# Kernel tuning notes

Measured on AMD Instinct MI355X. Metric: run time of the kernel, lower is better.

The kernel has to match this reference:

```python
import jax, jax.numpy as jnp
import numpy as np

N_NODES = 100000
N_EDGES = 1600000
N_HEADS = 4
D_IN = 128
D_OUT = 32


def setup_inputs() -> dict:
    key = jax.random.key(0)
    k1, k2, k3, k4, k5 = jax.random.split(key, 5)
    # glorot-ish scaling for params
    w_scale = (2.0 / (D_IN + D_OUT)) ** 0.5
    a_scale = (2.0 / (D_OUT + 1)) ** 0.5
    return {
        "H_in": jax.random.normal(k1, (N_NODES, D_IN), dtype=jnp.float32),
        "edge_index": jax.random.randint(k2, (2, N_EDGES), 0, N_NODES, dtype=jnp.int64),
        "W": jax.random.normal(k3, (N_HEADS, D_OUT, D_IN), dtype=jnp.float32) * w_scale,
        "A_src": jax.random.normal(k4, (N_HEADS, D_OUT), dtype=jnp.float32) * a_scale,
        "A_tgt": jax.random.normal(k5, (N_HEADS, D_OUT), dtype=jnp.float32) * a_scale,
    }


def reference(H_in, edge_index, W, A_src, A_tgt):
    # GATLayer.forward with dropout=0, skip=False, reduce='none', act=elu
    N = H_in.shape[0]
    src = edge_index[0]  # [E]
    tgt = edge_index[1]  # [E]

    # H_w: [N_h, N, D_out]  (einsum 'ij, nkj -> nik' in source)
    H_w = jnp.einsum("nd,hod->hno", H_in, W)

    # Per-node attention logit halves, then gather per edge (same math as
    # gathering features first and dotting with A afterwards).
    s_src = jnp.einsum("hno,ho->hn", H_w, A_src)  # [N_h, N]
    s_tgt = jnp.einsum("hno,ho->hn", H_w, A_tgt)  # [N_h, N]
    E_pre = s_src[:, src] + s_tgt[:, tgt]          # [N_h, E]
    E = jax.nn.leaky_relu(E_pre, negative_slope=0.2)

    # Segment softmax over edges grouped by target node (numerically stable).
    seg_max = jax.ops.segment_max(E.T, tgt, num_segments=N)  # [N, N_h]
    E_exp = jnp.exp(E - seg_max.T[:, tgt])                    # [N_h, E]
    seg_sum = jax.ops.segment_sum(E_exp.T, tgt, num_segments=N)  # [N, N_h]
    alpha = E_exp / seg_sum.T[:, tgt]                         # [N_h, E]

    # Weighted scatter-sum aggregation: msg [N_h, E, D_out] -> [N_h, N, D_out]
    msg = alpha[..., None] * H_w[:, src]
    H_out_pre = jax.vmap(lambda m: jax.ops.segment_sum(m, tgt, num_segments=N))(msg)

    return jax.nn.elu(H_out_pre)  # [N_h, N, D_out]
```

## Files before the change

### kernel.cpp

```cpp
#include <hip/hip_runtime.h>


#define CHUNK 4096
#define CAP 8192

typedef __attribute__((ext_vector_type(8))) short short8_t;
typedef __attribute__((ext_vector_type(4))) float float4v;
typedef __attribute__((ext_vector_type(2))) float float2v;

static __device__ inline float bf2f(unsigned short u) {
    return __uint_as_float(((unsigned int)u) << 16);
}
static __device__ inline unsigned short f2bf(float f) {
    unsigned int u = __float_as_uint(f);
    return (unsigned short)((u + 0x7fffu + ((u >> 16) & 1u)) >> 16);
}
static __device__ inline void splitf(float v, unsigned short& h, unsigned short& l) {
    unsigned short hb = f2bf(v);
    h = hb;
    l = f2bf(v - bf2f(hb));
}

__device__ inline int block_excl_scan(int v) {
    __shared__ int wsum[8];
    int lane = threadIdx.x & 63, w = threadIdx.x >> 6;
    int inc = v;
    for (int d = 1; d < 64; d <<= 1) {
        int t = __shfl_up(inc, d, 64);
        if (lane >= d) inc += t;
    }
    if (lane == 63) wsum[w] = inc;
    __syncthreads();
    int base = 0;
    for (int i = 0; i < w; ++i) base += wsum[i];
    __syncthreads();
    return base + inc - v;
}

__global__ __launch_bounds__(256) void k_scatA(const int* __restrict__ raw,
                                               int* __restrict__ cnt,
                                               unsigned int* __restrict__ pairs,
                                               int E, int N, int NB) {
    __shared__ unsigned int pl[CHUNK];
    __shared__ unsigned short bl[CHUNK];
    __shared__ int h[512];
    __shared__ int s_i64;
    const int tid = threadIdx.x;
    for (int i = tid; i < 512; i += 256) h[i] = 0;
    if (tid < 64) {
        unsigned int hiw = ((const unsigned int*)raw)[2 * tid + 1];
        unsigned long long b = __ballot(hiw == 0u);
        if (tid == 0) s_i64 = (__popcll(b) >= 32) ? 1 : 0;
    }
    __syncthreads();
    const bool i64 = s_i64 != 0;
    const int eBeg = blockIdx.x * CHUNK;
    const int eEnd = min(E, eBeg + CHUNK);
    const int cntE = eEnd - eBeg;
    for (int j = tid; j < cntE; j += 256) {
        int i = eBeg + j;
        int s, t;
        if (i64) {
            s = raw[2 * (size_t)i];
            t = raw[2 * ((size_t)E + i)];
        } else {
            s = raw[(size_t)i];
            t = raw[(size_t)E + i];
        }
        s = s < 0 ? 0 : (s >= N ? N - 1 : s);
        t = t < 0 ? 0 : (t >= N ? N - 1 : t);
        pl[j] = (unsigned)s | ((unsigned)(t & 255) << 24);
        int b = t >> 8;
        bl[j] = (unsigned short)b;
        atomicAdd(&h[b], 1);
    }
    __syncthreads();
    for (int b = tid; b < NB; b += 256) {
        int c = h[b];
        if (c > 0) h[b] = b * CAP + atomicAdd(&cnt[b], c);
    }
    __syncthreads();
    for (int j = tid; j < cntE; j += 256) {
        int slot = atomicAdd(&h[bl[j]], 1);
        pairs[slot] = pl[j];
    }
}

__global__ __launch_bounds__(256) void k_locs(const unsigned int* __restrict__ pairs,
                                              const int* __restrict__ cnt,
                                              int* __restrict__ offs,
                                              int* __restrict__ csr, int N, int NB,
                                              int E) {
    __shared__ int dcnt[256], cur[256];
    __shared__ int rsum[4];
    const int b = blockIdx.x;
    const int tid = threadIdx.x;

    int part = 0;
    for (int j = tid; j < b; j += 256) part += cnt[j];
    for (int d = 1; d < 64; d <<= 1) part += __shfl_xor(part, d, 64);
    if ((tid & 63) == 0) rsum[tid >> 6] = part;
    __syncthreads();
    const int obase = rsum[0] + rsum[1] + rsum[2] + rsum[3];

    const int c = cnt[b];
    const int rbeg = b * CAP;
    const int nodeBase = b << 8;
    dcnt[tid] = 0;
    __syncthreads();
    for (int i = tid; i < c; i += 256) atomicAdd(&dcnt[pairs[rbeg + i] >> 24], 1);
    __syncthreads();
    int v = dcnt[tid];
    int e = block_excl_scan(v);
    int n = nodeBase + tid;
    if (n < N) offs[n] = obase + e;
    cur[tid] = obase + e;
    __syncthreads();
    for (int i = tid; i < c; i += 256) {
        unsigned p = pairs[rbeg + i];
        int slot = atomicAdd(&cur[p >> 24], 1);
        csr[slot] = (int)(p & 0x00FFFFFFu);
    }
    if (b == 0 && tid == 0) offs[N] = E;
}

__global__ __launch_bounds__(256) void k_hw(const float* __restrict__ Hf,
                                            const float* __restrict__ Wf,
                                            const float* __restrict__ Asrc,
                                            const float* __restrict__ Atgt,
                                            unsigned short* __restrict__ Hwb,
                                            float* __restrict__ s_src,
                                            float* __restrict__ s_tgt, int nnodes) {
    __shared__ __align__(16) unsigned short Wh[64 * 136];
    __shared__ __align__(16) unsigned short Sh[16 * 136];
    __shared__ __align__(16) unsigned short Sl[16 * 136];
    __shared__ float sAs[128], sAt[128];

    int wave = threadIdx.x >> 6;
    int lane = threadIdx.x & 63;
    int mrow = lane & 15;
    int quad = lane >> 4;

    if (threadIdx.x < 128) {
        sAs[threadIdx.x] = Asrc[threadIdx.x];
        sAt[threadIdx.x] = Atgt[threadIdx.x];
    }
    __syncthreads();

    for (int i = threadIdx.x; i < 512; i += 256) {
        int r = i >> 5, c4 = (i & 31) * 4;
        float4v v = {0.f, 0.f, 0.f, 0.f};
        if (r < 8) {
            int hh_ = r & 3;
            const float* Ap = (r < 4) ? sAs : sAt;
            for (int o = 0; o < 32; ++o) {
                float4v w4 = *(const float4v*)(Wf + ((size_t)(hh_ * 32 + o)) * 128 + c4);
                float a = Ap[hh_ * 32 + o];
                v[0] += w4[0] * a;
                v[1] += w4[1] * a;
                v[2] += w4[2] * a;
                v[3] += w4[3] * a;
            }
        }
        ushort4 h4, l4;
        unsigned short hh, ll;
        splitf(v[0], hh, ll); h4.x = hh; l4.x = ll;
        splitf(v[1], hh, ll); h4.y = hh; l4.y = ll;
        splitf(v[2], hh, ll); h4.z = hh; l4.z = ll;
        splitf(v[3], hh, ll); h4.w = hh; l4.w = ll;
        *(ushort4*)&Sh[r * 136 + c4] = h4;
        *(ushort4*)&Sl[r * 136 + c4] = l4;
    }

    const float4v* wsrc = (const float4v*)Wf;

    for (int hb = 0; hb < 2; ++hb) {
        if (hb) __syncthreads();
        for (int i = threadIdx.x; i < 2048; i += 256) {
            int r = i >> 5, c4 = (i & 31) * 4;
            float4v v = wsrc[(hb * 64 + r) * 32 + (i & 31)];
            ushort4 h4;
            h4.x = f2bf(v[0]);
            h4.y = f2bf(v[1]);
            h4.z = f2bf(v[2]);
            h4.w = f2bf(v[3]);
            *(ushort4*)&Wh[r * 136 + c4] = h4;
        }
        __syncthreads();

        for (int nh = 0; nh < 2; ++nh) {
            int nbase = blockIdx.x * 128 + (wave * 2 + nh) * 16;
            if (nbase >= nnodes) continue;
            int anode = nbase + mrow;
            int nclamp = anode < nnodes ? anode : nnodes - 1;
            const float* Hp = Hf + (size_t)nclamp * 128 + quad * 8;

            float4v acc[4] = {};
            float4v accS = {};
            for (int kc = 0; kc < 4; ++kc) {
                float4v va = *(const float4v*)(Hp + kc * 32);
                float4v vb = *(const float4v*)(Hp + kc * 32 + 4);
                short8_t ah;
                ah[0] = (short)f2bf(va[0]);
                ah[1] = (short)f2bf(va[1]);
                ah[2] = (short)f2bf(va[2]);
                ah[3] = (short)f2bf(va[3]);
                ah[4] = (short)f2bf(vb[0]);
                ah[5] = (short)f2bf(vb[1]);
                ah[6] = (short)f2bf(vb[2]);
                ah[7] = (short)f2bf(vb[3]);
                for (int t = 0; t < 4; ++t) {
                    int boff = (t * 16 + mrow) * 136 + kc * 32 + quad * 8;
                    short8_t bh = *(const short8_t*)&Wh[boff];
                    acc[t] = __builtin_amdgcn_mfma_f32_16x16x32_bf16(ah, bh, acc[t], 0, 0, 0);
                }
                if (hb == 0) {
                    int soff = mrow * 136 + kc * 32 + quad * 8;
                    short8_t sh = *(const short8_t*)&Sh[soff];
                    short8_t sl = *(const short8_t*)&Sl[soff];
                    accS = __builtin_amdgcn_mfma_f32_16x16x32_bf16(ah, sh, accS, 0, 0, 0);
                    accS = __builtin_amdgcn_mfma_f32_16x16x32_bf16(ah, sl, accS, 0, 0, 0);
                }
            }
            for (int t = 0; t < 4; ++t)
                for (int r = 0; r < 4; ++r) {
                    int nrow = nbase + quad * 4 + r;
                    if (nrow < nnodes)
                        Hwb[(size_t)nrow * 128 + hb * 64 + t * 16 + mrow] = f2bf(acc[t][r]);
                }
            if (hb == 0) {
                for (int r = 0; r < 4; ++r) {
                    int nrow = nbase + quad * 4 + r;
                    if (nrow < nnodes) {
                        if (mrow < 4) s_src[nrow * 4 + mrow] = accS[r];
                        else if (mrow < 8) s_tgt[nrow * 4 + (mrow - 4)] = accS[r];
                    }
                }
            }
        }
    }
}

__global__ __launch_bounds__(256) void k_aggr(const int* __restrict__ offs,
                                              const int* __restrict__ csr,
                                              const float* __restrict__ s_src,
                                              const float* __restrict__ s_tgt,
                                              const unsigned int* __restrict__ Hwb,
                                              float* __restrict__ out, int nnodes) {
    __shared__ int srcs[4][64];
    __shared__ __align__(16) float wbuf[4][64 * 4];
    int wave = threadIdx.x >> 6, lane = threadIdx.x & 63;
    int n = blockIdx.x * 4 + wave;
    if (n >= nnodes) return;
    int off = offs[n];
    int deg = offs[n + 1] - off;
    int h = lane >> 4;

    const float4v* ss4 = (const float4v*)s_src;
    float4v st = ((const float4v*)s_tgt)[n];

    float se0 = 0.f, se1 = 0.f, se2 = 0.f, se3 = 0.f;
    float acc0 = 0.f, acc1 = 0.f;

    for (int base = 0; base < deg; base += 64) {
        int cnt = min(64, deg - base);
        asm volatile("s_waitcnt lgkmcnt(0)" ::: "memory");
        if (lane < cnt) {
            int s = csr[off + base + lane];
            srcs[wave][lane] = s;
            float4v ss = ss4[s];
            float4v w;
            for (int c = 0; c < 4; ++c) {
                float x = ss[c] + st[c];
                x = fminf(fmaxf(x, 0.2f * x), 60.f);
                w[c] = __expf(x);
            }
            se0 += w[0]; se1 += w[1]; se2 += w[2]; se3 += w[3];
            *(float4v*)&wbuf[wave][lane * 4] = w;
        }
        asm volatile("s_waitcnt lgkmcnt(0)" ::: "memory");

        int k = 0;
        for (; k + 8 <= cnt; k += 8) {
            int q0 = srcs[wave][k], q1 = srcs[wave][k + 1];
            int q2 = srcs[wave][k + 2], q3 = srcs[wave][k + 3];
            int q4 = srcs[wave][k + 4], q5 = srcs[wave][k + 5];
            int q6 = srcs[wave][k + 6], q7 = srcs[wave][k + 7];
            float w0 = wbuf[wave][k * 4 + h], w1 = wbuf[wave][(k + 1) * 4 + h];
            float w2 = wbuf[wave][(k + 2) * 4 + h], w3 = wbuf[wave][(k + 3) * 4 + h];
            float w4 = wbuf[wave][(k + 4) * 4 + h], w5 = wbuf[wave][(k + 5) * 4 + h];
            float w6 = wbuf[wave][(k + 6) * 4 + h], w7 = wbuf[wave][(k + 7) * 4 + h];
            unsigned int u0 = Hwb[(size_t)q0 * 64 + lane];
            unsigned int u1 = Hwb[(size_t)q1 * 64 + lane];
            unsigned int u2 = Hwb[(size_t)q2 * 64 + lane];
            unsigned int u3 = Hwb[(size_t)q3 * 64 + lane];
            unsigned int u4 = Hwb[(size_t)q4 * 64 + lane];
            unsigned int u5 = Hwb[(size_t)q5 * 64 + lane];
            unsigned int u6 = Hwb[(size_t)q6 * 64 + lane];
            unsigned int u7 = Hwb[(size_t)q7 * 64 + lane];
            acc0 += w0 * __uint_as_float(u0 << 16);
            acc1 += w0 * __uint_as_float(u0 & 0xffff0000u);
            acc0 += w1 * __uint_as_float(u1 << 16);
            acc1 += w1 * __uint_as_float(u1 & 0xffff0000u);
            acc0 += w2 * __uint_as_float(u2 << 16);
            acc1 += w2 * __uint_as_float(u2 & 0xffff0000u);
            acc0 += w3 * __uint_as_float(u3 << 16);
            acc1 += w3 * __uint_as_float(u3 & 0xffff0000u);
            acc0 += w4 * __uint_as_float(u4 << 16);
            acc1 += w4 * __uint_as_float(u4 & 0xffff0000u);
            acc0 += w5 * __uint_as_float(u5 << 16);
            acc1 += w5 * __uint_as_float(u5 & 0xffff0000u);
            acc0 += w6 * __uint_as_float(u6 << 16);
            acc1 += w6 * __uint_as_float(u6 & 0xffff0000u);
            acc0 += w7 * __uint_as_float(u7 << 16);
            acc1 += w7 * __uint_as_float(u7 & 0xffff0000u);
        }
        for (; k + 4 <= cnt; k += 4) {
            int q0 = srcs[wave][k], q1 = srcs[wave][k + 1];
            int q2 = srcs[wave][k + 2], q3 = srcs[wave][k + 3];
            float w0 = wbuf[wave][k * 4 + h], w1 = wbuf[wave][(k + 1) * 4 + h];
            float w2 = wbuf[wave][(k + 2) * 4 + h], w3 = wbuf[wave][(k + 3) * 4 + h];
            unsigned int u0 = Hwb[(size_t)q0 * 64 + lane];
            unsigned int u1 = Hwb[(size_t)q1 * 64 + lane];
            unsigned int u2 = Hwb[(size_t)q2 * 64 + lane];
            unsigned int u3 = Hwb[(size_t)q3 * 64 + lane];
            acc0 += w0 * __uint_as_float(u0 << 16);
            acc1 += w0 * __uint_as_float(u0 & 0xffff0000u);
            acc0 += w1 * __uint_as_float(u1 << 16);
            acc1 += w1 * __uint_as_float(u1 & 0xffff0000u);
            acc0 += w2 * __uint_as_float(u2 << 16);
            acc1 += w2 * __uint_as_float(u2 & 0xffff0000u);
            acc0 += w3 * __uint_as_float(u3 << 16);
            acc1 += w3 * __uint_as_float(u3 & 0xffff0000u);
        }
        for (; k < cnt; ++k) {
            int q = srcs[wave][k];
            float w = wbuf[wave][k * 4 + h];
            unsigned int u = Hwb[(size_t)q * 64 + lane];
            acc0 += w * __uint_as_float(u << 16);
            acc1 += w * __uint_as_float(u & 0xffff0000u);
        }
    }

    for (int d = 1; d < 64; d <<= 1) {
        se0 += __shfl_xor(se0, d, 64);
        se1 += __shfl_xor(se1, d, 64);
        se2 += __shfl_xor(se2, d, 64);
        se3 += __shfl_xor(se3, d, 64);
    }
    float seh = (h == 0) ? se0 : (h == 1) ? se1 : (h == 2) ? se2 : se3;
    float inv = seh > 0.f ? 1.0f / seh : 0.f;
    acc0 *= inv;
    acc1 *= inv;
    acc0 = acc0 > 0.f ? acc0 : __expf(acc0) - 1.0f;
    acc1 = acc1 > 0.f ? acc1 : __expf(acc1) - 1.0f;

    int o = (2 * lane) & 31;
    float2v val = {acc0, acc1};
    *(float2v*)&out[(((size_t)h * nnodes + n) * 32) + o] = val;
}

extern "C" void kernel_launch(void* const* d_in, const int* in_sizes, int n_in,
                              void* d_out, int out_size, void* d_ws, size_t ws_size,
                              hipStream_t stream) {
    const float* Hin = (const float*)d_in[0];
    const int* ei_raw = (const int*)d_in[1];
    const float* W = (const float*)d_in[2];
    const float* Asrc = (const float*)d_in[3];
    const float* Atgt = (const float*)d_in[4];
    int N = in_sizes[0] / 128;
    int E = in_sizes[1] / 2;
    int NB = (N + 255) >> 8;
    int nblkE = (E + CHUNK - 1) / CHUNK;

    char* ws = (char*)d_ws;
    size_t p = 0;
    auto alloc = [&](size_t bytes) {
        void* r = ws + p;
        p = (p + bytes + 511) & ~(size_t)511;
        return r;
    };
    unsigned short* Hwb = (unsigned short*)alloc((size_t)N * 128 * 2);
    float* s_src = (float*)alloc((size_t)N * 4 * 4);
    float* s_tgt = (float*)alloc((size_t)N * 4 * 4);
    int* offs = (int*)alloc((size_t)(N + 1) * 4);
    int* csr = (int*)alloc((size_t)E * 4);
    unsigned int* pairs = (unsigned int*)alloc((size_t)NB * CAP * 4);
    int* cnt = (int*)alloc((size_t)NB * 4);

    hipMemsetAsync(cnt, 0, (size_t)NB * 4, stream);
    k_scatA<<<dim3(nblkE), 256, 0, stream>>>(ei_raw, cnt, pairs, E, N, NB);
    k_locs<<<dim3(NB), 256, 0, stream>>>(pairs, cnt, offs, csr, N, NB, E);

    k_hw<<<dim3((N + 127) / 128), 256, 0, stream>>>(Hin, W, Asrc, Atgt, Hwb, s_src,
                                                    s_tgt, N);

    k_aggr<<<dim3((N + 3) / 4), 256, 0, stream>>>(offs, csr, s_src, s_tgt,
                                                  (const unsigned int*)Hwb,
                                                  (float*)d_out, N);
}
```

Measured before the change: 248.1 us.

## Precompute bf16 weights once and stream node projection without shared memory

A single-block prep kernel now converts W to bf16 and builds the split-bf16 attention projection vectors once, and also zeroes the bucket counters, which replaces the memset. The node projection kernel becomes 512-thread blocks where each wave handles one 16-node tile. It converts H to bf16 once and reads B fragments straight from global/L2 instead of staging W in LDS behind syncthreads. This removes per-block redundant weight conversion and barriers. The cost is a serial one-block launch and more global fragment loads.

```diff
diff --git a/kernel.cpp b/kernel.cpp
--- a/kernel.cpp
+++ b/kernel.cpp
@@ -35,6 +35,111 @@
     for (int i = 0; i < w; ++i) base += wsum[i];
     __syncthreads();
     return base + inc - v;
+}
+
+__global__ __launch_bounds__(256) void k_wprep(const float* __restrict__ Wf,
+                                               const float* __restrict__ Asrc,
+                                               const float* __restrict__ Atgt,
+                                               unsigned short* __restrict__ Wb,
+                                               unsigned short* __restrict__ Sgh,
+                                               unsigned short* __restrict__ Sgl,
+                                               int* __restrict__ cnt, int NB) {
+    __shared__ float As[128], At[128];
+    const int tid = threadIdx.x;
+    for (int i = tid; i < NB; i += 256) cnt[i] = 0;
+    if (tid < 128) {
+        As[tid] = Asrc[tid];
+        At[tid] = Atgt[tid];
+    }
+    __syncthreads();
+    for (int i = tid; i < 4096; i += 256) {
+        float4v v = ((const float4v*)Wf)[i];
+        ushort4 h4;
+        h4.x = f2bf(v[0]);
+        h4.y = f2bf(v[1]);
+        h4.z = f2bf(v[2]);
+        h4.w = f2bf(v[3]);
+        *(ushort4*)&Wb[i * 4] = h4;
+    }
+    for (int p = tid; p < 2048; p += 256) {
+        int r = p >> 7, k = p & 127;
+        float v = 0.f;
+        if (r < 8) {
+            int hh = r & 3;
+            const float* Ap = (r < 4) ? As : At;
+            for (int o = 0; o < 32; ++o)
+                v += Wf[((size_t)(hh * 32 + o)) * 128 + k] * Ap[hh * 32 + o];
+        }
+        unsigned short hh_, ll_;
+        splitf(v, hh_, ll_);
+        Sgh[p] = hh_;
+        Sgl[p] = ll_;
+    }
+}
+
+__global__ __launch_bounds__(512) void k_hw2(const float* __restrict__ Hf,
+                                             const unsigned short* __restrict__ Wb,
+                                             const unsigned short* __restrict__ Sgh,
+                                             const unsigned short* __restrict__ Sgl,
+                                             unsigned short* __restrict__ Hwb,
+                                             float* __restrict__ s_src,
+                                             float* __restrict__ s_tgt, int nnodes) {
+    int wave = threadIdx.x >> 6;
+    int lane = threadIdx.x & 63;
+    int mrow = lane & 15;
+    int quad = lane >> 4;
+    int nbase = blockIdx.x * 128 + wave * 16;
+    if (nbase >= nnodes) return;
+    int anode = nbase + mrow;
+    int nclamp = anode < nnodes ? anode : nnodes - 1;
+    const float* Hp = Hf + (size_t)nclamp * 128 + quad * 8;
+
+    short8_t ah[4];
+    for (int kc = 0; kc < 4; ++kc) {
+        float4v va = *(const float4v*)(Hp + kc * 32);
+        float4v vb = *(const float4v*)(Hp + kc * 32 + 4);
+        ah[kc][0] = (short)f2bf(va[0]);
+        ah[kc][1] = (short)f2bf(va[1]);
+        ah[kc][2] = (short)f2bf(va[2]);
+        ah[kc][3] = (short)f2bf(va[3]);
+        ah[kc][4] = (short)f2bf(vb[0]);
+        ah[kc][5] = (short)f2bf(vb[1]);
+        ah[kc][6] = (short)f2bf(vb[2]);
+        ah[kc][7] = (short)f2bf(vb[3]);
+    }
+
+    float4v accS = {};
+    for (int kc = 0; kc < 4; ++kc) {
+        short8_t sh = *(const short8_t*)&Sgh[mrow * 128 + kc * 32 + quad * 8];
+        short8_t sl = *(const short8_t*)&Sgl[mrow * 128 + kc * 32 + quad * 8];
+        accS = __builtin_amdgcn_mfma_f32_16x16x32_bf16(ah[kc], sh, accS, 0, 0, 0);
+        accS = __builtin_amdgcn_mfma_f32_16x16x32_bf16(ah[kc], sl, accS, 0, 0, 0);
+    }
+    for (int r = 0; r < 4; ++r) {
+        int nrow = nbase + quad * 4 + r;
+        if (nrow < nnodes) {
+            if (mrow < 4) s_src[nrow * 4 + mrow] = accS[r];
+            else if (mrow < 8) s_tgt[nrow * 4 + (mrow - 4)] = accS[r];
+        }
+    }
+
+    for (int hb = 0; hb < 2; ++hb) {
+        float4v acc[4] = {};
+        for (int kc = 0; kc < 4; ++kc) {
+#pragma unroll
+            for (int t = 0; t < 4; ++t) {
+                short8_t bh = *(const short8_t*)&Wb[(size_t)(hb * 64 + t * 16 + mrow) * 128 +
+                                                    kc * 32 + quad * 8];
+                acc[t] = __builtin_amdgcn_mfma_f32_16x16x32_bf16(ah[kc], bh, acc[t], 0, 0, 0);
+            }
+        }
+        for (int t = 0; t < 4; ++t)
+            for (int r = 0; r < 4; ++r) {
+                int nrow = nbase + quad * 4 + r;
+                if (nrow < nnodes)
+                    Hwb[(size_t)nrow * 128 + hb * 64 + t * 16 + mrow] = f2bf(acc[t][r]);
+            }
+    }
 }
 
 __global__ __launch_bounds__(256) void k_scatA(const int* __restrict__ raw,
@@ -122,123 +227,6 @@
         csr[slot] = (int)(p & 0x00FFFFFFu);
     }
     if (b == 0 && tid == 0) offs[N] = E;
-}
-
-__global__ __launch_bounds__(256) void k_hw(const float* __restrict__ Hf,
-                                            const float* __restrict__ Wf,
-                                            const float* __restrict__ Asrc,
-                                            const float* __restrict__ Atgt,
-                                            unsigned short* __restrict__ Hwb,
-                                            float* __restrict__ s_src,
-                                            float* __restrict__ s_tgt, int nnodes) {
-    __shared__ __align__(16) unsigned short Wh[64 * 136];
-    __shared__ __align__(16) unsigned short Sh[16 * 136];
-    __shared__ __align__(16) unsigned short Sl[16 * 136];
-    __shared__ float sAs[128], sAt[128];
-
-    int wave = threadIdx.x >> 6;
-    int lane = threadIdx.x & 63;
-    int mrow = lane & 15;
-    int quad = lane >> 4;
-
-    if (threadIdx.x < 128) {
-        sAs[threadIdx.x] = Asrc[threadIdx.x];
-        sAt[threadIdx.x] = Atgt[threadIdx.x];
-    }
-    __syncthreads();
-
-    for (int i = threadIdx.x; i < 512; i += 256) {
-        int r = i >> 5, c4 = (i & 31) * 4;
-        float4v v = {0.f, 0.f, 0.f, 0.f};
-        if (r < 8) {
-            int hh_ = r & 3;
-            const float* Ap = (r < 4) ? sAs : sAt;
-            for (int o = 0; o < 32; ++o) {
-                float4v w4 = *(const float4v*)(Wf + ((size_t)(hh_ * 32 + o)) * 128 + c4);
-                float a = Ap[hh_ * 32 + o];
-                v[0] += w4[0] * a;
-                v[1] += w4[1] * a;
-                v[2] += w4[2] * a;
-                v[3] += w4[3] * a;
-            }
-        }
-        ushort4 h4, l4;
-        unsigned short hh, ll;
-        splitf(v[0], hh, ll); h4.x = hh; l4.x = ll;
-        splitf(v[1], hh, ll); h4.y = hh; l4.y = ll;
-        splitf(v[2], hh, ll); h4.z = hh; l4.z = ll;
-        splitf(v[3], hh, ll); h4.w = hh; l4.w = ll;
-        *(ushort4*)&Sh[r * 136 + c4] = h4;
-        *(ushort4*)&Sl[r * 136 + c4] = l4;
-    }
-
-    const float4v* wsrc = (const float4v*)Wf;
-
-    for (int hb = 0; hb < 2; ++hb) {
-        if (hb) __syncthreads();
-        for (int i = threadIdx.x; i < 2048; i += 256) {
-            int r = i >> 5, c4 = (i & 31) * 4;
-            float4v v = wsrc[(hb * 64 + r) * 32 + (i & 31)];
-            ushort4 h4;
-            h4.x = f2bf(v[0]);
-            h4.y = f2bf(v[1]);
-            h4.z = f2bf(v[2]);
-            h4.w = f2bf(v[3]);
-            *(ushort4*)&Wh[r * 136 + c4] = h4;
-        }
-        __syncthreads();
-
-        for (int nh = 0; nh < 2; ++nh) {
-            int nbase = blockIdx.x * 128 + (wave * 2 + nh) * 16;
-            if (nbase >= nnodes) continue;
-            int anode = nbase + mrow;
-            int nclamp = anode < nnodes ? anode : nnodes - 1;
-            const float* Hp = Hf + (size_t)nclamp * 128 + quad * 8;
-
-            float4v acc[4] = {};
-            float4v accS = {};
-            for (int kc = 0; kc < 4; ++kc) {
-                float4v va = *(const float4v*)(Hp + kc * 32);
-                float4v vb = *(const float4v*)(Hp + kc * 32 + 4);
-                short8_t ah;
-                ah[0] = (short)f2bf(va[0]);
-                ah[1] = (short)f2bf(va[1]);
-                ah[2] = (short)f2bf(va[2]);
-                ah[3] = (short)f2bf(va[3]);
-                ah[4] = (short)f2bf(vb[0]);
-                ah[5] = (short)f2bf(vb[1]);
-                ah[6] = (short)f2bf(vb[2]);
-                ah[7] = (short)f2bf(vb[3]);
-                for (int t = 0; t < 4; ++t) {
-                    int boff = (t * 16 + mrow) * 136 + kc * 32 + quad * 8;
-                    short8_t bh = *(const short8_t*)&Wh[boff];
-                    acc[t] = __builtin_amdgcn_mfma_f32_16x16x32_bf16(ah, bh, acc[t], 0, 0, 0);
-                }
-                if (hb == 0) {
-                    int soff = mrow * 136 + kc * 32 + quad * 8;
-                    short8_t sh = *(const short8_t*)&Sh[soff];
-                    short8_t sl = *(const short8_t*)&Sl[soff];
-                    accS = __builtin_amdgcn_mfma_f32_16x16x32_bf16(ah, sh, accS, 0, 0, 0);
-                    accS = __builtin_amdgcn_mfma_f32_16x16x32_bf16(ah, sl, accS, 0, 0, 0);
-                }
-            }
-            for (int t = 0; t < 4; ++t)
-                for (int r = 0; r < 4; ++r) {
-                    int nrow = nbase + quad * 4 + r;
-                    if (nrow < nnodes)
-                        Hwb[(size_t)nrow * 128 + hb * 64 + t * 16 + mrow] = f2bf(acc[t][r]);
-                }
-            if (hb == 0) {
-                for (int r = 0; r < 4; ++r) {
-                    int nrow = nbase + quad * 4 + r;
-                    if (nrow < nnodes) {
-                        if (mrow < 4) s_src[nrow * 4 + mrow] = accS[r];
-                        else if (mrow < 8) s_tgt[nrow * 4 + (mrow - 4)] = accS[r];
-                    }
-                }
-            }
-        }
-    }
 }
 
 __global__ __launch_bounds__(256) void k_aggr(const int* __restrict__ offs,
@@ -387,13 +375,15 @@
     int* csr = (int*)alloc((size_t)E * 4);
     unsigned int* pairs = (unsigned int*)alloc((size_t)NB * CAP * 4);
     int* cnt = (int*)alloc((size_t)NB * 4);
-
-    hipMemsetAsync(cnt, 0, (size_t)NB * 4, stream);
+    unsigned short* Wb = (unsigned short*)alloc(128 * 128 * 2);
+    unsigned short* Sgh = (unsigned short*)alloc(16 * 128 * 2);
+    unsigned short* Sgl = (unsigned short*)alloc(16 * 128 * 2);
+
+    k_wprep<<<dim3(1), 256, 0, stream>>>(W, Asrc, Atgt, Wb, Sgh, Sgl, cnt, NB);
+    k_hw2<<<dim3((N + 127) / 128), 512, 0, stream>>>(Hin, Wb, Sgh, Sgl, Hwb, s_src,
+                                                     s_tgt, N);
     k_scatA<<<dim3(nblkE), 256, 0, stream>>>(ei_raw, cnt, pairs, E, N, NB);
     k_locs<<<dim3(NB), 256, 0, stream>>>(pairs, cnt, offs, csr, N, NB, E);
-
-    k_hw<<<dim3((N + 127) / 128), 256, 0, stream>>>(Hin, W, Asrc, Atgt, Hwb, s_src,
-                                                    s_tgt, N);
 
     k_aggr<<<dim3((N + 3) / 4), 256, 0, stream>>>(offs, csr, s_src, s_tgt,
                                                   (const unsigned int*)Hwb,
```

New measurement: 390.7 us. 1.57x slower.
